# Kernel tuning notes

Hardware: AMD Instinct MI355X
Metric: run time of the kernel (lower is better)

Reference implementation:

```python
import jax, jax.numpy as jnp
import numpy as np

B, D, N, H = 2, 512, 2048, 8
DK = D // H
EPS = 1e-5


def conv1x1(x, w, b):
    # kernel-size-1 Conv1d == channel-mixing GEMM: (o,i) x (b,i,n) -> (b,o,n)
    return jnp.einsum('oi,bin->bon', w, x) + b[None, :, None]


def setup_inputs() -> dict:
    key = jax.random.key(0)
    ks = jax.random.split(key, 20)
    s = 0.02
    return {
        'init_query': jax.random.normal(ks[0], (B, D, N), jnp.float32),
        'key_t': jax.random.normal(ks[1], (B, D, N), jnp.float32),
        'value': jax.random.normal(ks[2], (B, D, N), jnp.float32),
        'mask': jax.random.randint(ks[3], (B, 1, N, N), 0, 2, jnp.int32),
        'Wq': jax.random.normal(ks[4], (D, D), jnp.float32) * s,
        'bq': jax.random.normal(ks[5], (D,), jnp.float32) * s,
        'Wk': jax.random.normal(ks[6], (D, D), jnp.float32) * s,
        'bk': jax.random.normal(ks[7], (D,), jnp.float32) * s,
        'Wv': jax.random.normal(ks[8], (D, D), jnp.float32) * s,
        'bv': jax.random.normal(ks[9], (D,), jnp.float32) * s,
        'Wm': jax.random.normal(ks[10], (D, D), jnp.float32) * s,
        'bm': jax.random.normal(ks[11], (D,), jnp.float32) * s,
        'W1': jax.random.normal(ks[12], (2 * D, 2 * D), jnp.float32) * s,
        'b1': jax.random.normal(ks[13], (2 * D,), jnp.float32) * s,
        'gamma': jnp.ones((2 * D,), jnp.float32),
        'beta': jnp.zeros((2 * D,), jnp.float32),
        'rmean': jax.random.normal(ks[14], (2 * D,), jnp.float32) * s,
        'rvar': jnp.abs(jax.random.normal(ks[15], (2 * D,), jnp.float32)) * 0.1 + 0.5,
        'W2': jax.random.normal(ks[16], (D, 2 * D), jnp.float32) * s,
        'b2': jnp.zeros((D,), jnp.float32),  # nn.init.constant_(bias, 0.0)
    }


def reference(init_query, key_t, value, mask, Wq, bq, Wk, bk, Wv, bv, Wm, bm,
              W1, b1, gamma, beta, rmean, rvar, W2, b2):
    # projections, split channels into (d_k, n_heads) exactly like torch .view
    q = conv1x1(init_query, Wq, bq).reshape(B, DK, H, N)
    k = conv1x1(key_t, Wk, bk).reshape(B, DK, H, N)
    v = conv1x1(value, Wv, bv).reshape(B, DK, H, N)
    scores = jnp.einsum('bdhn,bdhm->bhnm', q, k) / jnp.sqrt(jnp.float32(DK))
    scores = jnp.where(mask == 0, jnp.float32(-1e9), scores)
    attn = jax.nn.softmax(scores, axis=-1)
    x = jnp.einsum('bhnm,bdhm->bdhn', attn, v).reshape(B, D, N)
    x = conv1x1(x, Wm, bm)
    x = jnp.concatenate([x, init_query], axis=1)  # (B, 2D, N)
    h = conv1x1(x, W1, b1)
    # BatchNorm1d (inference mode with running stats) + ReLU
    h = (h - rmean[None, :, None]) * (gamma / jnp.sqrt(rvar + EPS))[None, :, None] + beta[None, :, None]
    h = jax.nn.relu(h)
    return conv1x1(h, W2, b2)
```

## Files before the change

kernel.cpp:

```cpp
#include <hip/hip_runtime.h>

typedef unsigned short u16;
typedef unsigned int u32;
typedef unsigned long long u64;
typedef long long i64;
typedef __bf16 bf16x8 __attribute__((ext_vector_type(8)));
typedef u16 u16x8 __attribute__((ext_vector_type(8)));
typedef u32 u32x2 __attribute__((ext_vector_type(2)));
typedef float f32x4 __attribute__((ext_vector_type(4)));

#define DEV __device__ __forceinline__

constexpr int BB = 2, DD = 512, NN = 2048, HH = 8, DKc = 64, D2 = 1024;

constexpr float QSC = 0.125f * 1.44269504088896340736f;

constexpr i64 OFF_CAT = 0;
constexpr i64 OFF_XKT = 8388608;
constexpr i64 OFF_XVT = 12582912;
constexpr i64 OFF_HT  = 8388608;
constexpr i64 OFF_QH  = 16777216;
constexpr i64 OFF_KH  = 20971520;
constexpr i64 OFF_VT  = 25165824;
constexpr i64 OFF_WQP = 29360128;
constexpr i64 OFF_WKP = 29884416;
constexpr i64 OFF_WVP = 30408704;
constexpr i64 OFF_WMT = 30932992;
constexpr i64 OFF_W1A = 31457280;
constexpr i64 OFF_W1C = 32505856;
constexpr i64 OFF_W2B = 34603008;
constexpr i64 OFF_BQP = 35651584;
constexpr i64 OFF_BKP = 35653632;
constexpr i64 OFF_BVP = 35655680;
constexpr i64 OFF_BNA = 35657728;
constexpr i64 OFF_BNC = 35661824;
constexpr i64 OFF_LP  = 35665920;
constexpr i64 OFF_MSK = 35928064;

DEV u16 f2bf(float f) {
  u32 u = __float_as_uint(f);
  u = u + 0x7FFFu + ((u >> 16) & 1u);
  return (u16)(u >> 16);
}

DEV float bf2f(u16 u) { return __uint_as_float(((u32)u) << 16); }

DEV u32 packbf(float lo, float hi) {
  return __builtin_amdgcn_perm(__float_as_uint(hi), __float_as_uint(lo), 0x07060302u);
}

DEV float fexp2(float x) {
#if __has_builtin(__builtin_amdgcn_exp2f)
  return __builtin_amdgcn_exp2f(x);
#else
  return exp2f(x);
#endif
}

DEV bf16x8 ldfrag(const u16* p) {
  bf16x8 v;
  __builtin_memcpy(&v, __builtin_assume_aligned(p, 16), 16);
  return v;
}

DEV bf16x8 ldfrag8(const u16* p) {
  bf16x8 v;
  __builtin_memcpy(&v, __builtin_assume_aligned(p, 8), 16);
  return v;
}

DEV bf16x8 ones8() {
  u16x8 u = {0x3F80, 0x3F80, 0x3F80, 0x3F80, 0x3F80, 0x3F80, 0x3F80, 0x3F80};
  bf16x8 v;
  __builtin_memcpy(&v, &u, 16);
  return v;
}

DEV void gload16(const void* g, void* lds) {
  __builtin_amdgcn_global_load_lds((__attribute__((address_space(1))) void*)g,
                                   (__attribute__((address_space(3))) void*)lds, 16, 0, 0);
}

DEV f32x4 mfma16(bf16x8 a, bf16x8 b, f32x4 c) {
  return __builtin_amdgcn_mfma_f32_16x16x32_bf16(a, b, c, 0, 0, 0);
}

__global__ __launch_bounds__(256) void prep_kernel(
    const float* __restrict__ Wq, const float* __restrict__ Wk, const float* __restrict__ Wv,
    const float* __restrict__ Wm, const float* __restrict__ W1, const float* __restrict__ W2,
    const float* __restrict__ bq, const float* __restrict__ bk, const float* __restrict__ bv,
    const float* __restrict__ bm, const float* __restrict__ b1, const float* __restrict__ gamma_,
    const float* __restrict__ beta_, const float* __restrict__ rmean,
    const float* __restrict__ rvar, const int* __restrict__ mask,
    u16* __restrict__ wqp, u16* __restrict__ wkp, u16* __restrict__ wvp, u16* __restrict__ wmt,
    u16* __restrict__ w1a, u16* __restrict__ w1c, u16* __restrict__ w2b,
    float* __restrict__ bqp, float* __restrict__ bkp, float* __restrict__ bvp,
    float* __restrict__ bna, float* __restrict__ bnc, u32* __restrict__ mw) {
  const int blk = blockIdx.x, t = threadIdx.x;
  if (blk < 768) {
    const int which = blk >> 8, lb = blk & 255;
    const float* W = which == 0 ? Wq : (which == 1 ? Wk : Wv);
    u16* dst = which == 0 ? wqp : (which == 1 ? wkp : wvp);
    for (int e = lb * 256 + t; e < 262144; e += 65536) {
      int op = e >> 9, i = e & 511;
      int dk = op & 63, h = op >> 6;
      dst[e] = f2bf(W[(dk * 8 + h) * 512 + i]);
    }
  } else if (blk < 1024) {
    const int lb = blk - 768;
    for (int e = lb * 256 + t; e < 262144; e += 65536) {
      int cp = e >> 9, o = e & 511;
      int dk = cp & 63, h = cp >> 6;
      wmt[e] = f2bf(Wm[o * 512 + dk * 8 + h]);
    }
  } else if (blk < 1280) {
    const int lb = blk - 1024;
    for (int e = lb * 256 + t; e < 524288; e += 65536) {
      int row = e >> 9, o = e & 511;
      w1a[e] = f2bf(W1[(i64)row * 1024 + o]);
    }
  } else if (blk < 1536) {
    const int lb = blk - 1280;
    for (int e = lb * 256 + t; e < 524288; e += 65536) {
      int row = e >> 9, j = e & 511;
      w1c[(i64)row * 1024 + 512 + j] = f2bf(W1[(i64)row * 1024 + 512 + j]);
    }
  } else if (blk < 1792) {
    const int lb = blk - 1536;
    for (int e = lb * 256 + t; e < 524288; e += 65536) w2b[e] = f2bf(W2[e]);
  } else if (blk < 1808) {
    __shared__ float sm[4][64];
    const int base = (blk - 1792) * 64;
    const int el = t & 63, oq = t >> 6;
    const float* wrow = W1 + (i64)(base + el) * 1024 + oq * 128;
    const float* bmq = bm + oq * 128;
    float s = 0.f;
#pragma unroll 8
    for (int j = 0; j < 128; j += 4) {
      float4 x = *(const float4*)(wrow + j);
      float4 y = *(const float4*)(bmq + j);
      s += x.x * y.x + x.y * y.y + x.z * y.z + x.w * y.w;
    }
    sm[oq][el] = s;
    __syncthreads();
    if (t < 64) {
      int e = base + t;
      float a = gamma_[e] * rsqrtf(rvar[e] + 1e-5f);
      bna[e] = a;
      bnc[e] = (b1[e] - rmean[e]) * a + beta_[e] + a * (sm[0][t] + sm[1][t] + sm[2][t] + sm[3][t]);
    }
  } else if (blk == 1808) {
    for (int e = t; e < 512; e += 256) {
      int src = (e & 63) * 8 + (e >> 6);
      bqp[e] = bq[src]; bkp[e] = bk[src]; bvp[e] = bv[src];
    }
  } else {
    const int tid = (blk - 1809) * 256 + t;
    const i64 base = (i64)tid * 32;
    const int4* mp = (const int4*)(mask + base);
    u32 word = 0;
#pragma unroll
    for (int j = 0; j < 8; ++j) {
      int4 x = mp[j];
      u32 nib = (x.x != 0 ? 1u : 0u) | (x.y != 0 ? 2u : 0u) | (x.z != 0 ? 4u : 0u) |
                (x.w != 0 ? 8u : 0u);
      word |= nib << (j * 4);
    }
    mw[tid] = word;
  }
}

__global__ __launch_bounds__(256) void transpose_cvt(const float* __restrict__ iq,
                                                     const float* __restrict__ kt,
                                                     const float* __restrict__ vv,
                                                     u16* __restrict__ cat, u16* __restrict__ xkt,
                                                     u16* __restrict__ xvt) {
  __shared__ float tile[32][33];
  const int z = blockIdx.z, tensor = z >> 1, b = z & 1;
  const float* src = tensor == 0 ? iq : (tensor == 1 ? kt : vv);
  src += (i64)b * DD * NN;
  u16* dst; i64 ldd; int coff;
  if (tensor == 0)      { dst = cat + (i64)b * NN * D2; ldd = D2; coff = DD; }
  else if (tensor == 1) { dst = xkt + (i64)b * NN * DD; ldd = DD; coff = 0; }
  else                  { dst = xvt + (i64)b * NN * DD; ldd = DD; coff = 0; }
  const int x0 = blockIdx.x * 32, y0 = blockIdx.y * 32;
  const int col = threadIdx.x & 31, rg = threadIdx.x >> 5;
#pragma unroll
  for (int i = 0; i < 4; ++i) {
    int row = rg + i * 8;
    tile[row][col] = src[(i64)(y0 + row) * NN + x0 + col];
  }
  __syncthreads();
  const int dp = threadIdx.x & 15, rbase = threadIdx.x >> 4;
  u32* dst32 = (u32*)dst;
  const i64 ldw = ldd >> 1;
  const int cw = (coff + y0) >> 1;
#pragma unroll
  for (int i = 0; i < 2; ++i) {
    int rr = rbase + i * 16;
    dst32[(i64)(x0 + rr) * ldw + cw + dp] = packbf(tile[2 * dp][rr], tile[2 * dp + 1][rr]);
  }
}

template <int AM, int AN>
DEV void gemm_core(const u16* __restrict__ A, i64 lda, const u16* __restrict__ Bp, i64 ldb,
                   int K, u16* As, u16* Bs, f32x4 (&acc)[AM][AN]) {
  constexpr int BM = AM * 32, BN = AN * 32;
  const int t = threadIdx.x, w = t >> 6, l = t & 63, quad = l >> 4, l15 = l & 15;
  const int wm = (w >> 1) * AM * 16, wn = (w & 1) * AN * 16;
  for (int kk = 0; kk < K; kk += 64) {
    __syncthreads();
#pragma unroll
    for (int j = 0; j < BM / 32; ++j) {
      int ch = j * 256 + w * 64 + l, r = ch >> 3, c = ch & 7;
      gload16(A + (i64)r * lda + kk + ((c ^ (r & 7)) << 3), As + (j * 256 + w * 64) * 8);
    }
#pragma unroll
    for (int j = 0; j < BN / 32; ++j) {
      int ch = j * 256 + w * 64 + l, r = ch >> 3, c = ch & 7;
      gload16(Bp + (i64)r * ldb + kk + ((c ^ (r & 7)) << 3), Bs + (j * 256 + w * 64) * 8);
    }
    __syncthreads();
#pragma unroll
    for (int kc = 0; kc < 2; ++kc) {
      const int sw = ((kc * 4 + quad) ^ (l15 & 7)) << 3;
      bf16x8 af[AM], bfr[AN];
#pragma unroll
      for (int i = 0; i < AM; ++i) af[i] = ldfrag(&As[(wm + i * 16 + l15) * 64 + sw]);
#pragma unroll
      for (int j = 0; j < AN; ++j) bfr[j] = ldfrag(&Bs[(wn + j * 16 + l15) * 64 + sw]);
#pragma unroll
      for (int i = 0; i < AM; ++i)
#pragma unroll
        for (int j = 0; j < AN; ++j) acc[i][j] = mfma16(af[i], bfr[j], acc[i][j]);
    }
  }
}

__global__ __launch_bounds__(256) void qkv_gemm(const u16* __restrict__ cat,
                                                const u16* __restrict__ xkt,
                                                const u16* __restrict__ xvt,
                                                const u16* __restrict__ wqp,
                                                const u16* __restrict__ wkp,
                                                const u16* __restrict__ wvp,
                                                const float* __restrict__ bqp,
                                                const float* __restrict__ bkp,
                                                const float* __restrict__ bvp,
                                                u16* __restrict__ qh, u16* __restrict__ kh,
                                                u16* __restrict__ vt) {
  __shared__ __align__(16) u16 As[128 * 64];
  __shared__ __align__(16) u16 Bs[64 * 64];
  const int z = blockIdx.z, op = z >> 1, b = z & 1;
  const int t = threadIdx.x, w = t >> 6, l = t & 63, quad = l >> 4, l15 = l & 15;
  const int wm = (w >> 1) * 64, wn = (w & 1) * 32;
  int mx, ny;
  const u16 *A, *Bp;
  i64 lda, ldb;
  if (op < 2) {
    mx = blockIdx.x; ny = blockIdx.y;
    A = (op == 0 ? cat + DD : xkt);
    lda = (op == 0 ? D2 : DD);
    A += (i64)b * NN * lda + (i64)mx * 128 * lda;
    Bp = (op == 0 ? wqp : wkp) + (i64)ny * 64 * DD;
    ldb = DD;
  } else {
    int f = blockIdx.x * 8 + blockIdx.y;
    mx = f >> 5; ny = f & 31;
    A = wvp + (i64)mx * 128 * DD; lda = DD;
    Bp = xvt + (i64)b * NN * DD + (i64)ny * 64 * DD; ldb = DD;
  }
  f32x4 acc[4][2] = {};
  gemm_core<4, 2>(A, lda, Bp, ldb, DD, As, Bs, acc);

  const int rowBase = mx * 128 + wm + quad * 4;
  const int colBase = ny * 64 + wn + l15;
  if (op < 2) {
    const float* bias = (op == 0 ? bqp : bkp);
    const float sc = (op == 0 ? QSC : 1.f);
    u16* dst = (op == 0 ? qh : kh) + (i64)b * HH * NN * DKc;
#pragma unroll
    for (int j = 0; j < 2; ++j) {
      const int col = colBase + j * 16;
      const float cA = bias[col];
#pragma unroll
      for (int i = 0; i < 4; ++i)
#pragma unroll
        for (int r = 0; r < 4; ++r) {
          const int row = rowBase + i * 16 + r;
          dst[(i64)(col >> 6) * (NN * 64) + (i64)row * 64 + (col & 63)] =
              f2bf((acc[i][j][r] + cA) * sc);
        }
    }
  } else {
    u16* dst = vt + (i64)b * HH * DKc * NN;
#pragma unroll
    for (int j = 0; j < 2; ++j) {
      const int col = colBase + j * 16;
      const int colp = (col & ~63) | (((col & 15) << 2) | ((col >> 4) & 3));
#pragma unroll
      for (int i = 0; i < 4; ++i)
#pragma unroll
        for (int r = 0; r < 4; ++r) {
          const int row = rowBase + i * 16 + r;
          dst[(i64)row * NN + colp] = f2bf(acc[i][j][r] + bvp[row]);
        }
    }
  }
}

struct GArgs {
  const u16* A; i64 lda, sAb;
  const u16* B; i64 ldb, sBb;
  void* C; i64 ldc, sCb;
  const float* p1; const float* p2;
  int K;
};

template <int MODE, int AM, int AN>
__global__ __launch_bounds__(256) void gemm_bt(GArgs g) {
  __shared__ __align__(16) u16 As[AM * 32 * 64];
  __shared__ __align__(16) u16 Bs[AN * 32 * 64];
  const int t = threadIdx.x, w = t >> 6, l = t & 63, quad = l >> 4, l15 = l & 15;
  const int wm = (w >> 1) * AM * 16, wn = (w & 1) * AN * 16;
  const int bz = blockIdx.z;
  const u16* A = g.A + (i64)bz * g.sAb + (i64)blockIdx.x * (AM * 32) * g.lda;
  const u16* Bp = g.B + (i64)bz * g.sBb + (i64)blockIdx.y * (AN * 32) * g.ldb;
  f32x4 acc[AM][AN] = {};
  gemm_core<AM, AN>(A, g.lda, Bp, g.ldb, g.K, As, Bs, acc);

  const int rowBase = blockIdx.x * (AM * 32) + wm + quad * 4;
  const int colBase = blockIdx.y * (AN * 32) + wn + l15;
#pragma unroll
  for (int j = 0; j < AN; ++j) {
    const int col = colBase + j * 16;
    float cA = 0.f, cB = 0.f;
    if (MODE == 3) { cA = g.p1[col]; cB = g.p2[col]; }
#pragma unroll
    for (int i = 0; i < AM; ++i) {
#pragma unroll
      for (int r = 0; r < 4; ++r) {
        const int row = rowBase + i * 16 + r;
        float v = acc[i][j][r];
        if (MODE == 3) {
          float x = v * cA + cB;
          ((u16*)g.C + (i64)bz * g.sCb)[(i64)row * g.ldc + col] = f2bf(x > 0.f ? x : 0.f);
        } else if (MODE == 4) {
          ((float*)g.C + (i64)bz * g.sCb)[(i64)row * g.ldc + col] = v + g.p1[row];
        } else {
          ((u16*)g.C + (i64)bz * g.sCb)[(i64)row * g.ldc + col] = f2bf(v);
        }
      }
    }
  }
}

__global__ __launch_bounds__(256) void flash_attn(const u16* __restrict__ Qh,
                                                  const u16* __restrict__ Kh,
                                                  const u16* __restrict__ Vt,
                                                  const u64* __restrict__ MW,
                                                  u16* __restrict__ Opart,
                                                  float* __restrict__ Lp) {
  __shared__ __align__(16) u16 Qs[64 * 64];
  __shared__ __align__(16) u16 Ks[64 * 64];
  __shared__ __align__(16) u16 Vs[64 * 64];
  __shared__ __align__(16) u16 Ps[4][16 * 68];
  const int t = threadIdx.x, w = t >> 6, l = t & 63, quad = l >> 4, l15 = l & 15;
  const int nt = blockIdx.x, h = blockIdx.y, b = blockIdx.z >> 1, sp = blockIdx.z & 1;
  const u16* Qb = Qh + ((i64)(b * HH + h) * NN + nt * 64) * 64;
  const u16* Kb = Kh + (i64)(b * HH + h) * NN * 64;
  const u16* Vb = Vt + (i64)(b * HH + h) * 64 * NN;
  const bf16x8 ONE = ones8();
#pragma unroll
  for (int j = 0; j < 2; ++j) {
    int ch = j * 256 + w * 64 + l, r = ch >> 3, c = ch & 7;
    gload16(Qb + r * 64 + ((c ^ (r & 7)) << 3), &Qs[(j * 256 + w * 64) * 8]);
  }
  __syncthreads();
  bf16x8 qf[2];
#pragma unroll
  for (int kc = 0; kc < 2; ++kc)
    qf[kc] = ldfrag(&Qs[(w * 16 + l15) * 64 + (((kc * 4 + quad) ^ (l15 & 7)) << 3)]);

  f32x4 oacc[4] = {};
  f32x4 lacc = {};
  const int mt0 = sp * 16, mt1 = mt0 + 16;
  for (int mt = mt0; mt < mt1; ++mt) {
    __syncthreads();
#pragma unroll
    for (int j = 0; j < 2; ++j) {
      int ch = j * 256 + w * 64 + l, r = ch >> 3, c = ch & 7;
      gload16(Kb + (i64)mt * 4096 + r * 64 + ((c ^ (r & 7)) << 3), &Ks[(j * 256 + w * 64) * 8]);
      gload16(Vb + (i64)r * NN + mt * 64 + ((c ^ (r & 7)) << 3), &Vs[(j * 256 + w * 64) * 8]);
    }
    __syncthreads();
    f32x4 s[4];
#pragma unroll
    for (int ct = 0; ct < 4; ++ct) {
      const int sw = l15 & 7;
      bf16x8 k0 = ldfrag(&Ks[(ct * 16 + l15) * 64 + ((quad ^ sw) << 3)]);
      bf16x8 k1 = ldfrag(&Ks[(ct * 16 + l15) * 64 + (((4 + quad) ^ sw) << 3)]);
      f32x4 z = {};
      z = mfma16(qf[0], k0, z);
      z = mfma16(qf[1], k1, z);
      s[ct] = z;
    }
#pragma unroll
    for (int r = 0; r < 4; ++r) {
      int n = nt * 64 + w * 16 + quad * 4 + r;
      u64 sh = MW[(i64)(b * NN + n) * 32 + mt] >> l15;
      u32 m01 = ((u32)sh & 0x00010001u) * 0xFFFFu;
      u32 m23 = ((u32)(sh >> 32) & 0x00010001u) * 0xFFFFu;
      u32 w0 = packbf(fexp2(s[0][r]), fexp2(s[1][r])) & m01;
      u32 w1 = packbf(fexp2(s[2][r]), fexp2(s[3][r])) & m23;
      u32x2 pair = {w0, w1};
      __builtin_memcpy(__builtin_assume_aligned(&Ps[w][(quad * 4 + r) * 68 + l15 * 4], 8), &pair, 8);
    }
    asm volatile("" ::: "memory");
    bf16x8 pf0 = ldfrag8(&Ps[w][l15 * 68 + quad * 8]);
    bf16x8 pf1 = ldfrag8(&Ps[w][l15 * 68 + 32 + quad * 8]);
    lacc = mfma16(pf0, ONE, lacc);
    lacc = mfma16(pf1, ONE, lacc);
#pragma unroll
    for (int dt = 0; dt < 4; ++dt) {
      const int sw = l15 & 7;
      bf16x8 v0 = ldfrag(&Vs[(dt * 16 + l15) * 64 + ((quad ^ sw) << 3)]);
      bf16x8 v1 = ldfrag(&Vs[(dt * 16 + l15) * 64 + (((4 + quad) ^ sw) << 3)]);
      oacc[dt] = mfma16(pf0, v0, oacc[dt]);
      oacc[dt] = mfma16(pf1, v1, oacc[dt]);
    }
  }
  u16* Op = Opart + (i64)sp * BB * NN * DD;
#pragma unroll
  for (int dt = 0; dt < 4; ++dt)
#pragma unroll
    for (int r = 0; r < 4; ++r) {
      int n = nt * 64 + w * 16 + quad * 4 + r;
      Op[((i64)b * NN + n) * DD + h * DKc + dt * 16 + l15] = f2bf(oacc[dt][r]);
    }
  if (l15 == 0) {
#pragma unroll
    for (int r = 0; r < 4; ++r) {
      int n = nt * 64 + w * 16 + quad * 4 + r;
      Lp[((i64)(sp * BB + b) * HH + h) * NN + n] = lacc[r];
    }
  }
}

__global__ __launch_bounds__(256) void combine(const u16* __restrict__ Opart,
                                               const float* __restrict__ Lp,
                                               u16* __restrict__ cat) {
  const int tid = blockIdx.x * 256 + threadIdx.x;
  const int b = tid >> 18, rem = tid & 262143;
  const int n = rem >> 7, cq = rem & 127;
  const int c0 = cq << 2, h = c0 >> 6;
  const u16* p0 = Opart + ((i64)b * NN + n) * DD + c0;
  const u16* p1 = p0 + (i64)BB * NN * DD;
  u16 a0[4], a1[4];
  __builtin_memcpy(a0, __builtin_assume_aligned(p0, 8), 8);
  __builtin_memcpy(a1, __builtin_assume_aligned(p1, 8), 8);
  float l0 = Lp[((i64)b * HH + h) * NN + n];
  float l1 = Lp[((i64)(BB + b) * HH + h) * NN + n];
  float rl = __builtin_amdgcn_rcpf(l0 + l1);
  u16 o[4];
#pragma unroll
  for (int j = 0; j < 4; ++j) o[j] = f2bf((bf2f(a0[j]) + bf2f(a1[j])) * rl);
  __builtin_memcpy(__builtin_assume_aligned(&cat[((i64)b * NN + n) * D2 + c0], 8), o, 8);
}

extern "C" void kernel_launch(void* const* d_in, const int* in_sizes, int n_in,
                              void* d_out, int out_size, void* d_ws, size_t ws_size,
                              hipStream_t stream) {
  (void)in_sizes; (void)n_in; (void)out_size; (void)ws_size;
  const float* iq    = (const float*)d_in[0];
  const float* kt    = (const float*)d_in[1];
  const float* vv    = (const float*)d_in[2];
  const int*   mask  = (const int*)d_in[3];
  const float* Wq    = (const float*)d_in[4];
  const float* bq    = (const float*)d_in[5];
  const float* Wk    = (const float*)d_in[6];
  const float* bk    = (const float*)d_in[7];
  const float* Wv    = (const float*)d_in[8];
  const float* bv    = (const float*)d_in[9];
  const float* Wm    = (const float*)d_in[10];
  const float* bm    = (const float*)d_in[11];
  const float* W1    = (const float*)d_in[12];
  const float* b1    = (const float*)d_in[13];
  const float* gamma_= (const float*)d_in[14];
  const float* beta_ = (const float*)d_in[15];
  const float* rmean = (const float*)d_in[16];
  const float* rvar  = (const float*)d_in[17];
  const float* W2    = (const float*)d_in[18];
  const float* b2    = (const float*)d_in[19];

  char* ws = (char*)d_ws;
  u16* cat = (u16*)(ws + OFF_CAT);
  u16* xkt = (u16*)(ws + OFF_XKT);
  u16* xvt = (u16*)(ws + OFF_XVT);
  u16* ht  = (u16*)(ws + OFF_HT);
  u16* qh  = (u16*)(ws + OFF_QH);
  u16* kh  = (u16*)(ws + OFF_KH);
  u16* vt  = (u16*)(ws + OFF_VT);
  u16* wqp = (u16*)(ws + OFF_WQP);
  u16* wkp = (u16*)(ws + OFF_WKP);
  u16* wvp = (u16*)(ws + OFF_WVP);
  u16* wmt = (u16*)(ws + OFF_WMT);
  u16* w1a = (u16*)(ws + OFF_W1A);
  u16* w1c = (u16*)(ws + OFF_W1C);
  u16* w2b = (u16*)(ws + OFF_W2B);
  float* bqp = (float*)(ws + OFF_BQP);
  float* bkp = (float*)(ws + OFF_BKP);
  float* bvp = (float*)(ws + OFF_BVP);
  float* bna = (float*)(ws + OFF_BNA);
  float* bnc = (float*)(ws + OFF_BNC);
  float* lp  = (float*)(ws + OFF_LP);
  u32* mw = (u32*)(ws + OFF_MSK);
  u16* opart = (u16*)(ws + OFF_XKT);

  prep_kernel<<<2833, 256, 0, stream>>>(Wq, Wk, Wv, Wm, W1, W2, bq, bk, bv, bm, b1, gamma_,
                                        beta_, rmean, rvar, mask, wqp, wkp, wvp, wmt, w1a, w1c,
                                        w2b, bqp, bkp, bvp, bna, bnc, mw);
  transpose_cvt<<<dim3(64, 16, 6), 256, 0, stream>>>(iq, kt, vv, cat, xkt, xvt);

  GArgs ca{w1a, DD, 0, wmt, DD, 0, w1c, D2, 0, nullptr, nullptr, DD};
  gemm_bt<5, 4, 2><<<dim3(8, 8, 1), 256, 0, stream>>>(ca);

  qkv_gemm<<<dim3(16, 8, 6), 256, 0, stream>>>(cat, xkt, xvt, wqp, wkp, wvp, bqp, bkp, bvp,
                                               qh, kh, vt);

  flash_attn<<<dim3(32, 8, 4), 256, 0, stream>>>(qh, kh, vt, (const u64*)mw, opart, lp);
  combine<<<2048, 256, 0, stream>>>(opart, lp, cat);

  GArgs wa{cat, D2, (i64)NN * D2, w1c, D2, 0, ht, D2, (i64)NN * D2, bna, bnc, D2};
  gemm_bt<3, 4, 2><<<dim3(16, 16, 2), 256, 0, stream>>>(wa);
  GArgs w2a{w2b, D2, 0, ht, D2, (i64)NN * D2, d_out, NN, (i64)DD * NN, b2, nullptr, D2};
  gemm_bt<4, 2, 2><<<dim3(8, 32, 2), 256, 0, stream>>>(w2a);
}
```

Before: 237.9 us.

## Merge prep kernels, fold Wm·W1 GEMM into QKV launch, use 32x32 MFMA attention with 4-way split

Fuses the prep and transpose kernels into a single launch, and folds the W1·Wm weight-composition GEMM into the QKV GEMM launch as an extra z-slice. Flash attention is rewritten to use 32x32x16 MFMA with 128-row query tiles, Q fragments loaded straight from global memory, and a 4-way KV split. The mask bitpacking and V column permutation are changed to match the new fragment layout, and the combine kernel now sums four partials. The workspace is re-laid out so the partial outputs no longer alias the transposed inputs, and the W1 GEMM tile shape is changed. The goal is fewer launches and higher MFMA efficiency, at the cost of more partial-output traffic and a strided mask gather.

```diff
diff --git a/kernel.cpp b/kernel.cpp
--- a/kernel.cpp
+++ b/kernel.cpp
@@ -6,8 +6,8 @@
 typedef long long i64;
 typedef __bf16 bf16x8 __attribute__((ext_vector_type(8)));
 typedef u16 u16x8 __attribute__((ext_vector_type(8)));
-typedef u32 u32x2 __attribute__((ext_vector_type(2)));
 typedef float f32x4 __attribute__((ext_vector_type(4)));
+typedef float f32x16 __attribute__((ext_vector_type(16)));
 
 #define DEV __device__ __forceinline__
 
@@ -15,27 +15,29 @@
 
 constexpr float QSC = 0.125f * 1.44269504088896340736f;
 
+constexpr i64 MB = 1048576;
 constexpr i64 OFF_CAT = 0;
-constexpr i64 OFF_XKT = 8388608;
-constexpr i64 OFF_XVT = 12582912;
-constexpr i64 OFF_HT  = 8388608;
-constexpr i64 OFF_QH  = 16777216;
-constexpr i64 OFF_KH  = 20971520;
-constexpr i64 OFF_VT  = 25165824;
-constexpr i64 OFF_WQP = 29360128;
-constexpr i64 OFF_WKP = 29884416;
-constexpr i64 OFF_WVP = 30408704;
-constexpr i64 OFF_WMT = 30932992;
-constexpr i64 OFF_W1A = 31457280;
-constexpr i64 OFF_W1C = 32505856;
-constexpr i64 OFF_W2B = 34603008;
-constexpr i64 OFF_BQP = 35651584;
-constexpr i64 OFF_BKP = 35653632;
-constexpr i64 OFF_BVP = 35655680;
-constexpr i64 OFF_BNA = 35657728;
-constexpr i64 OFF_BNC = 35661824;
-constexpr i64 OFF_LP  = 35665920;
-constexpr i64 OFF_MSK = 35928064;
+constexpr i64 OFF_XKT = 8 * MB;
+constexpr i64 OFF_XVT = 12 * MB;
+constexpr i64 OFF_QH  = 16 * MB;
+constexpr i64 OFF_KH  = 20 * MB;
+constexpr i64 OFF_VT  = 24 * MB;
+constexpr i64 OFF_HT  = 28 * MB;
+constexpr i64 OFF_OP  = 36 * MB;
+constexpr i64 OFF_LP  = 68 * MB;
+constexpr i64 OFF_WQP = 69 * MB;
+constexpr i64 OFF_WKP = 69 * MB + 524288;
+constexpr i64 OFF_WVP = 69 * MB + 1048576;
+constexpr i64 OFF_WMT = 69 * MB + 1572864;
+constexpr i64 OFF_W1A = 71 * MB;
+constexpr i64 OFF_W1C = 72 * MB;
+constexpr i64 OFF_W2B = 74 * MB;
+constexpr i64 OFF_BQP = 75 * MB;
+constexpr i64 OFF_BKP = 75 * MB + 2048;
+constexpr i64 OFF_BVP = 75 * MB + 4096;
+constexpr i64 OFF_BNA = 75 * MB + 8192;
+constexpr i64 OFF_BNC = 75 * MB + 12288;
+constexpr i64 OFF_MSK = 76 * MB;
 
 DEV u16 f2bf(float f) {
   u32 u = __float_as_uint(f);
@@ -85,17 +87,24 @@
   return __builtin_amdgcn_mfma_f32_16x16x32_bf16(a, b, c, 0, 0, 0);
 }
 
-__global__ __launch_bounds__(256) void prep_kernel(
+DEV f32x16 mfma32(bf16x8 a, bf16x8 b, f32x16 c) {
+  return __builtin_amdgcn_mfma_f32_32x32x16_bf16(a, b, c, 0, 0, 0);
+}
+
+__global__ __launch_bounds__(256) void prep_all(
     const float* __restrict__ Wq, const float* __restrict__ Wk, const float* __restrict__ Wv,
     const float* __restrict__ Wm, const float* __restrict__ W1, const float* __restrict__ W2,
     const float* __restrict__ bq, const float* __restrict__ bk, const float* __restrict__ bv,
     const float* __restrict__ bm, const float* __restrict__ b1, const float* __restrict__ gamma_,
     const float* __restrict__ beta_, const float* __restrict__ rmean,
     const float* __restrict__ rvar, const int* __restrict__ mask,
+    const float* __restrict__ iq, const float* __restrict__ kt, const float* __restrict__ vv,
     u16* __restrict__ wqp, u16* __restrict__ wkp, u16* __restrict__ wvp, u16* __restrict__ wmt,
     u16* __restrict__ w1a, u16* __restrict__ w1c, u16* __restrict__ w2b,
     float* __restrict__ bqp, float* __restrict__ bkp, float* __restrict__ bvp,
-    float* __restrict__ bna, float* __restrict__ bnc, u32* __restrict__ mw) {
+    float* __restrict__ bna, float* __restrict__ bnc, u32* __restrict__ mw,
+    u16* __restrict__ cat, u16* __restrict__ xkt, u16* __restrict__ xvt) {
+  __shared__ float tile[32][33];
   const int blk = blockIdx.x, t = threadIdx.x;
   if (blk < 768) {
     const int which = blk >> 8, lb = blk & 255;
@@ -154,51 +163,44 @@
       int src = (e & 63) * 8 + (e >> 6);
       bqp[e] = bq[src]; bkp[e] = bk[src]; bvp[e] = bv[src];
     }
+  } else if (blk < 2833) {
+    const int tid = (blk - 1809) * 256 + t;
+    const int l = tid & 63, mt = (tid >> 6) & 31, g = (tid >> 11) & 63, b = tid >> 17;
+    const int kv0 = mt * 64 + (l & 31);
+    u32 word = 0;
+#pragma unroll
+    for (int reg = 0; reg < 16; ++reg) {
+      int r = (reg & 3) + 8 * (reg >> 2) + 4 * (l >> 5);
+      const int* mp = mask + ((i64)b * NN + g * 32 + r) * NN + kv0;
+      word |= (mp[0] != 0 ? (1u << (2 * reg)) : 0u) | (mp[32] != 0 ? (2u << (2 * reg)) : 0u);
+    }
+    mw[tid] = word;
   } else {
-    const int tid = (blk - 1809) * 256 + t;
-    const i64 base = (i64)tid * 32;
-    const int4* mp = (const int4*)(mask + base);
-    u32 word = 0;
-#pragma unroll
-    for (int j = 0; j < 8; ++j) {
-      int4 x = mp[j];
-      u32 nib = (x.x != 0 ? 1u : 0u) | (x.y != 0 ? 2u : 0u) | (x.z != 0 ? 4u : 0u) |
-                (x.w != 0 ? 8u : 0u);
-      word |= nib << (j * 4);
-    }
-    mw[tid] = word;
-  }
-}
-
-__global__ __launch_bounds__(256) void transpose_cvt(const float* __restrict__ iq,
-                                                     const float* __restrict__ kt,
-                                                     const float* __restrict__ vv,
-                                                     u16* __restrict__ cat, u16* __restrict__ xkt,
-                                                     u16* __restrict__ xvt) {
-  __shared__ float tile[32][33];
-  const int z = blockIdx.z, tensor = z >> 1, b = z & 1;
-  const float* src = tensor == 0 ? iq : (tensor == 1 ? kt : vv);
-  src += (i64)b * DD * NN;
-  u16* dst; i64 ldd; int coff;
-  if (tensor == 0)      { dst = cat + (i64)b * NN * D2; ldd = D2; coff = DD; }
-  else if (tensor == 1) { dst = xkt + (i64)b * NN * DD; ldd = DD; coff = 0; }
-  else                  { dst = xvt + (i64)b * NN * DD; ldd = DD; coff = 0; }
-  const int x0 = blockIdx.x * 32, y0 = blockIdx.y * 32;
-  const int col = threadIdx.x & 31, rg = threadIdx.x >> 5;
-#pragma unroll
-  for (int i = 0; i < 4; ++i) {
-    int row = rg + i * 8;
-    tile[row][col] = src[(i64)(y0 + row) * NN + x0 + col];
-  }
-  __syncthreads();
-  const int dp = threadIdx.x & 15, rbase = threadIdx.x >> 4;
-  u32* dst32 = (u32*)dst;
-  const i64 ldw = ldd >> 1;
-  const int cw = (coff + y0) >> 1;
-#pragma unroll
-  for (int i = 0; i < 2; ++i) {
-    int rr = rbase + i * 16;
-    dst32[(i64)(x0 + rr) * ldw + cw + dp] = packbf(tile[2 * dp][rr], tile[2 * dp + 1][rr]);
+    const int idx = blk - 2833;
+    const int bx = idx & 63, by = (idx >> 6) & 15, bz = idx >> 10;
+    const int tensor = bz >> 1, b = bz & 1;
+    const float* src = (tensor == 0 ? iq : (tensor == 1 ? kt : vv)) + (i64)b * DD * NN;
+    u16* dst; i64 ldd; int coff;
+    if (tensor == 0)      { dst = cat + (i64)b * NN * D2; ldd = D2; coff = DD; }
+    else if (tensor == 1) { dst = xkt + (i64)b * NN * DD; ldd = DD; coff = 0; }
+    else                  { dst = xvt + (i64)b * NN * DD; ldd = DD; coff = 0; }
+    const int x0 = bx * 32, y0 = by * 32;
+    const int col = t & 31, rg = t >> 5;
+#pragma unroll
+    for (int i = 0; i < 4; ++i) {
+      int row = rg + i * 8;
+      tile[row][col] = src[(i64)(y0 + row) * NN + x0 + col];
+    }
+    __syncthreads();
+    const int dp = t & 15, rbase = t >> 4;
+    u32* dst32 = (u32*)dst;
+    const i64 ldw = ldd >> 1;
+    const int cw = (coff + y0) >> 1;
+#pragma unroll
+    for (int i = 0; i < 2; ++i) {
+      int rr = rbase + i * 16;
+      dst32[(i64)(x0 + rr) * ldw + cw + dp] = packbf(tile[2 * dp][rr], tile[2 * dp + 1][rr]);
+    }
   }
 }
 
@@ -243,14 +245,17 @@
                                                 const u16* __restrict__ wqp,
                                                 const u16* __restrict__ wkp,
                                                 const u16* __restrict__ wvp,
+                                                const u16* __restrict__ w1a,
+                                                const u16* __restrict__ wmt,
                                                 const float* __restrict__ bqp,
                                                 const float* __restrict__ bkp,
                                                 const float* __restrict__ bvp,
                                                 u16* __restrict__ qh, u16* __restrict__ kh,
-                                                u16* __restrict__ vt) {
+                                                u16* __restrict__ vt, u16* __restrict__ w1c) {
   __shared__ __align__(16) u16 As[128 * 64];
   __shared__ __align__(16) u16 Bs[64 * 64];
-  const int z = blockIdx.z, op = z >> 1, b = z & 1;
+  const int z = blockIdx.z, b = z & 1;
+  const int op = (z == 6) ? 3 : (z >> 1);
   const int t = threadIdx.x, w = t >> 6, l = t & 63, quad = l >> 4, l15 = l & 15;
   const int wm = (w >> 1) * 64, wn = (w & 1) * 32;
   int mx, ny;
@@ -263,11 +268,16 @@
     A += (i64)b * NN * lda + (i64)mx * 128 * lda;
     Bp = (op == 0 ? wqp : wkp) + (i64)ny * 64 * DD;
     ldb = DD;
-  } else {
+  } else if (op == 2) {
     int f = blockIdx.x * 8 + blockIdx.y;
     mx = f >> 5; ny = f & 31;
     A = wvp + (i64)mx * 128 * DD; lda = DD;
     Bp = xvt + (i64)b * NN * DD + (i64)ny * 64 * DD; ldb = DD;
+  } else {
+    if (blockIdx.x >= 8) return;
+    mx = blockIdx.x; ny = blockIdx.y;
+    A = w1a + (i64)mx * 128 * DD; lda = DD;
+    Bp = wmt + (i64)ny * 64 * DD; ldb = DD;
   }
   f32x4 acc[4][2] = {};
   gemm_core<4, 2>(A, lda, Bp, ldb, DD, As, Bs, acc);
@@ -291,18 +301,30 @@
               f2bf((acc[i][j][r] + cA) * sc);
         }
     }
-  } else {
+  } else if (op == 2) {
     u16* dst = vt + (i64)b * HH * DKc * NN;
 #pragma unroll
     for (int j = 0; j < 2; ++j) {
       const int col = colBase + j * 16;
-      const int colp = (col & ~63) | (((col & 15) << 2) | ((col >> 4) & 3));
+      const int colp = (col & ~63) | (((col & 31) << 1) | ((col >> 5) & 1));
 #pragma unroll
       for (int i = 0; i < 4; ++i)
 #pragma unroll
         for (int r = 0; r < 4; ++r) {
           const int row = rowBase + i * 16 + r;
           dst[(i64)row * NN + colp] = f2bf(acc[i][j][r] + bvp[row]);
+        }
+    }
+  } else {
+#pragma unroll
+    for (int j = 0; j < 2; ++j) {
+      const int col = colBase + j * 16;
+#pragma unroll
+      for (int i = 0; i < 4; ++i)
+#pragma unroll
+        for (int r = 0; r < 4; ++r) {
+          const int row = rowBase + i * 16 + r;
+          w1c[(i64)row * D2 + col] = f2bf(acc[i][j][r]);
         }
     }
   }
@@ -344,10 +366,8 @@
         if (MODE == 3) {
           float x = v * cA + cB;
           ((u16*)g.C + (i64)bz * g.sCb)[(i64)row * g.ldc + col] = f2bf(x > 0.f ? x : 0.f);
-        } else if (MODE == 4) {
+        } else {
           ((float*)g.C + (i64)bz * g.sCb)[(i64)row * g.ldc + col] = v + g.p1[row];
-        } else {
-          ((u16*)g.C + (i64)bz * g.sCb)[(i64)row * g.ldc + col] = f2bf(v);
         }
       }
     }
@@ -357,92 +377,79 @@
 __global__ __launch_bounds__(256) void flash_attn(const u16* __restrict__ Qh,
                                                   const u16* __restrict__ Kh,
                                                   const u16* __restrict__ Vt,
-                                                  const u64* __restrict__ MW,
+                                                  const u32* __restrict__ MW2,
                                                   u16* __restrict__ Opart,
                                                   float* __restrict__ Lp) {
-  __shared__ __align__(16) u16 Qs[64 * 64];
   __shared__ __align__(16) u16 Ks[64 * 64];
   __shared__ __align__(16) u16 Vs[64 * 64];
-  __shared__ __align__(16) u16 Ps[4][16 * 68];
-  const int t = threadIdx.x, w = t >> 6, l = t & 63, quad = l >> 4, l15 = l & 15;
-  const int nt = blockIdx.x, h = blockIdx.y, b = blockIdx.z >> 1, sp = blockIdx.z & 1;
-  const u16* Qb = Qh + ((i64)(b * HH + h) * NN + nt * 64) * 64;
+  __shared__ __align__(16) u16 Ps[4][32 * 68];
+  const int t = threadIdx.x, w = t >> 6, l = t & 63, l31 = l & 31, lh = l >> 5;
+  const int nt = blockIdx.x, h = blockIdx.y, b = blockIdx.z >> 2, sp = blockIdx.z & 3;
+  const u16* Qb = Qh + ((i64)(b * HH + h) * NN + nt * 128 + w * 32) * 64;
   const u16* Kb = Kh + (i64)(b * HH + h) * NN * 64;
   const u16* Vb = Vt + (i64)(b * HH + h) * 64 * NN;
+  const u32* MWb = MW2 + ((i64)(b * 64 + nt * 4 + w) * 32) * 64 + l;
   const bf16x8 ONE = ones8();
-#pragma unroll
-  for (int j = 0; j < 2; ++j) {
-    int ch = j * 256 + w * 64 + l, r = ch >> 3, c = ch & 7;
-    gload16(Qb + r * 64 + ((c ^ (r & 7)) << 3), &Qs[(j * 256 + w * 64) * 8]);
-  }
-  __syncthreads();
-  bf16x8 qf[2];
-#pragma unroll
-  for (int kc = 0; kc < 2; ++kc)
-    qf[kc] = ldfrag(&Qs[(w * 16 + l15) * 64 + (((kc * 4 + quad) ^ (l15 & 7)) << 3)]);
-
-  f32x4 oacc[4] = {};
-  f32x4 lacc = {};
-  const int mt0 = sp * 16, mt1 = mt0 + 16;
-  for (int mt = mt0; mt < mt1; ++mt) {
+  bf16x8 qf[4];
+#pragma unroll
+  for (int kc = 0; kc < 4; ++kc)
+    __builtin_memcpy(&qf[kc], Qb + (i64)l31 * 64 + kc * 16 + lh * 8, 16);
+
+  f32x16 oacc0 = {}, oacc1 = {}, lacc = {};
+  for (int mt = sp * 8; mt < sp * 8 + 8; ++mt) {
     __syncthreads();
 #pragma unroll
     for (int j = 0; j < 2; ++j) {
-      int ch = j * 256 + w * 64 + l, r = ch >> 3, c = ch & 7;
-      gload16(Kb + (i64)mt * 4096 + r * 64 + ((c ^ (r & 7)) << 3), &Ks[(j * 256 + w * 64) * 8]);
-      gload16(Vb + (i64)r * NN + mt * 64 + ((c ^ (r & 7)) << 3), &Vs[(j * 256 + w * 64) * 8]);
+      int ch = j * 256 + t, r = ch >> 3, c = ch & 7;
+      gload16(Kb + (i64)(mt * 64 + r) * 64 + ((c ^ (r & 7)) << 3), &Ks[ch * 8]);
+      gload16(Vb + (i64)r * NN + mt * 64 + ((c ^ (r & 7)) << 3), &Vs[ch * 8]);
     }
     __syncthreads();
-    f32x4 s[4];
-#pragma unroll
-    for (int ct = 0; ct < 4; ++ct) {
-      const int sw = l15 & 7;
-      bf16x8 k0 = ldfrag(&Ks[(ct * 16 + l15) * 64 + ((quad ^ sw) << 3)]);
-      bf16x8 k1 = ldfrag(&Ks[(ct * 16 + l15) * 64 + (((4 + quad) ^ sw) << 3)]);
-      f32x4 z = {};
-      z = mfma16(qf[0], k0, z);
-      z = mfma16(qf[1], k1, z);
-      s[ct] = z;
-    }
-#pragma unroll
-    for (int r = 0; r < 4; ++r) {
-      int n = nt * 64 + w * 16 + quad * 4 + r;
-      u64 sh = MW[(i64)(b * NN + n) * 32 + mt] >> l15;
-      u32 m01 = ((u32)sh & 0x00010001u) * 0xFFFFu;
-      u32 m23 = ((u32)(sh >> 32) & 0x00010001u) * 0xFFFFu;
-      u32 w0 = packbf(fexp2(s[0][r]), fexp2(s[1][r])) & m01;
-      u32 w1 = packbf(fexp2(s[2][r]), fexp2(s[3][r])) & m23;
-      u32x2 pair = {w0, w1};
-      __builtin_memcpy(__builtin_assume_aligned(&Ps[w][(quad * 4 + r) * 68 + l15 * 4], 8), &pair, 8);
+    f32x16 s0 = {}, s1 = {};
+#pragma unroll
+    for (int kc = 0; kc < 4; ++kc) {
+      const int r1 = 32 + l31;
+      bf16x8 k0 = ldfrag(&Ks[l31 * 64 + (((kc * 2 + lh) ^ (l31 & 7)) << 3)]);
+      bf16x8 k1 = ldfrag(&Ks[r1 * 64 + (((kc * 2 + lh) ^ (r1 & 7)) << 3)]);
+      s0 = mfma32(qf[kc], k0, s0);
+      s1 = mfma32(qf[kc], k1, s1);
+    }
+    const u32 mword = MWb[(i64)mt * 64];
+#pragma unroll
+    for (int reg = 0; reg < 16; ++reg) {
+      const int row = (reg & 3) + 8 * (reg >> 2) + 4 * lh;
+      u32 sh = mword >> (2 * reg);
+      u32 m01 = ((sh & 1u) | ((sh & 2u) << 15)) * 0xFFFFu;
+      u32 pv = packbf(fexp2(s0[reg]), fexp2(s1[reg])) & m01;
+      *(u32*)__builtin_assume_aligned(&Ps[w][row * 68 + l31 * 2], 4) = pv;
     }
     asm volatile("" ::: "memory");
-    bf16x8 pf0 = ldfrag8(&Ps[w][l15 * 68 + quad * 8]);
-    bf16x8 pf1 = ldfrag8(&Ps[w][l15 * 68 + 32 + quad * 8]);
-    lacc = mfma16(pf0, ONE, lacc);
-    lacc = mfma16(pf1, ONE, lacc);
-#pragma unroll
-    for (int dt = 0; dt < 4; ++dt) {
-      const int sw = l15 & 7;
-      bf16x8 v0 = ldfrag(&Vs[(dt * 16 + l15) * 64 + ((quad ^ sw) << 3)]);
-      bf16x8 v1 = ldfrag(&Vs[(dt * 16 + l15) * 64 + (((4 + quad) ^ sw) << 3)]);
-      oacc[dt] = mfma16(pf0, v0, oacc[dt]);
-      oacc[dt] = mfma16(pf1, v1, oacc[dt]);
-    }
-  }
-  u16* Op = Opart + (i64)sp * BB * NN * DD;
-#pragma unroll
-  for (int dt = 0; dt < 4; ++dt)
-#pragma unroll
-    for (int r = 0; r < 4; ++r) {
-      int n = nt * 64 + w * 16 + quad * 4 + r;
-      Op[((i64)b * NN + n) * DD + h * DKc + dt * 16 + l15] = f2bf(oacc[dt][r]);
-    }
-  if (l15 == 0) {
-#pragma unroll
-    for (int r = 0; r < 4; ++r) {
-      int n = nt * 64 + w * 16 + quad * 4 + r;
-      Lp[((i64)(sp * BB + b) * HH + h) * NN + n] = lacc[r];
-    }
+    bf16x8 pf[4];
+#pragma unroll
+    for (int kc = 0; kc < 4; ++kc) pf[kc] = ldfrag8(&Ps[w][l31 * 68 + kc * 16 + lh * 8]);
+#pragma unroll
+    for (int kc = 0; kc < 4; ++kc) lacc = mfma32(pf[kc], ONE, lacc);
+#pragma unroll
+    for (int kc = 0; kc < 4; ++kc) {
+      const int r1 = 32 + l31;
+      bf16x8 v0 = ldfrag(&Vs[l31 * 64 + (((kc * 2 + lh) ^ (l31 & 7)) << 3)]);
+      bf16x8 v1 = ldfrag(&Vs[r1 * 64 + (((kc * 2 + lh) ^ (r1 & 7)) << 3)]);
+      oacc0 = mfma32(pf[kc], v0, oacc0);
+      oacc1 = mfma32(pf[kc], v1, oacc1);
+    }
+  }
+  u16* Op = Opart + (i64)sp * (BB * NN * DD) + ((i64)b * NN + nt * 128 + w * 32) * DD + h * 64;
+#pragma unroll
+  for (int reg = 0; reg < 16; ++reg) {
+    const int row = (reg & 3) + 8 * (reg >> 2) + 4 * lh;
+    Op[(i64)row * DD + l31] = f2bf(oacc0[reg]);
+    Op[(i64)row * DD + 32 + l31] = f2bf(oacc1[reg]);
+  }
+  if (l31 == 0) {
+    float* Lpb = Lp + ((i64)(sp * BB + b) * HH + h) * NN + nt * 128 + w * 32;
+#pragma unroll
+    for (int reg = 0; reg < 16; ++reg)
+      Lpb[(reg & 3) + 8 * (reg >> 2) + 4 * lh] = lacc[reg];
   }
 }
 
@@ -453,17 +460,22 @@
   const int b = tid >> 18, rem = tid & 262143;
   const int n = rem >> 7, cq = rem & 127;
   const int c0 = cq << 2, h = c0 >> 6;
-  const u16* p0 = Opart + ((i64)b * NN + n) * DD + c0;
-  const u16* p1 = p0 + (i64)BB * NN * DD;
-  u16 a0[4], a1[4];
-  __builtin_memcpy(a0, __builtin_assume_aligned(p0, 8), 8);
-  __builtin_memcpy(a1, __builtin_assume_aligned(p1, 8), 8);
-  float l0 = Lp[((i64)b * HH + h) * NN + n];
-  float l1 = Lp[((i64)(BB + b) * HH + h) * NN + n];
-  float rl = __builtin_amdgcn_rcpf(l0 + l1);
+  const i64 base = ((i64)b * NN + n) * DD + c0;
+  const i64 stride = (i64)BB * NN * DD;
+  float acc[4] = {0.f, 0.f, 0.f, 0.f};
+  float lsum = 0.f;
+#pragma unroll
+  for (int s = 0; s < 4; ++s) {
+    u16 a[4];
+    __builtin_memcpy(a, __builtin_assume_aligned(Opart + s * stride + base, 8), 8);
+#pragma unroll
+    for (int j = 0; j < 4; ++j) acc[j] += bf2f(a[j]);
+    lsum += Lp[((i64)(s * BB + b) * HH + h) * NN + n];
+  }
+  float rl = __builtin_amdgcn_rcpf(lsum);
   u16 o[4];
 #pragma unroll
-  for (int j = 0; j < 4; ++j) o[j] = f2bf((bf2f(a0[j]) + bf2f(a1[j])) * rl);
+  for (int j = 0; j < 4; ++j) o[j] = f2bf(acc[j] * rl);
   __builtin_memcpy(__builtin_assume_aligned(&cat[((i64)b * NN + n) * D2 + c0], 8), o, 8);
 }
 
@@ -496,10 +508,12 @@
   u16* cat = (u16*)(ws + OFF_CAT);
   u16* xkt = (u16*)(ws + OFF_XKT);
   u16* xvt = (u16*)(ws + OFF_XVT);
-  u16* ht  = (u16*)(ws + OFF_HT);
   u16* qh  = (u16*)(ws + OFF_QH);
   u16* kh  = (u16*)(ws + OFF_KH);
   u16* vt  = (u16*)(ws + OFF_VT);
+  u16* ht  = (u16*)(ws + OFF_HT);
+  u16* opart = (u16*)(ws + OFF_OP);
+  float* lp  = (float*)(ws + OFF_LP);
   u16* wqp = (u16*)(ws + OFF_WQP);
   u16* wkp = (u16*)(ws + OFF_WKP);
   u16* wvp = (u16*)(ws + OFF_WVP);
@@ -512,26 +526,17 @@
   float* bvp = (float*)(ws + OFF_BVP);
   float* bna = (float*)(ws + OFF_BNA);
   float* bnc = (float*)(ws + OFF_BNC);
-  float* lp  = (float*)(ws + OFF_LP);
   u32* mw = (u32*)(ws + OFF_MSK);
-  u16* opart = (u16*)(ws + OFF_XKT);
-
-  prep_kernel<<<2833, 256, 0, stream>>>(Wq, Wk, Wv, Wm, W1, W2, bq, bk, bv, bm, b1, gamma_,
-                                        beta_, rmean, rvar, mask, wqp, wkp, wvp, wmt, w1a, w1c,
-                                        w2b, bqp, bkp, bvp, bna, bnc, mw);
-  transpose_cvt<<<dim3(64, 16, 6), 256, 0, stream>>>(iq, kt, vv, cat, xkt, xvt);
-
-  GArgs ca{w1a, DD, 0, wmt, DD, 0, w1c, D2, 0, nullptr, nullptr, DD};
-  gemm_bt<5, 4, 2><<<dim3(8, 8, 1), 256, 0, stream>>>(ca);
-
-  qkv_gemm<<<dim3(16, 8, 6), 256, 0, stream>>>(cat, xkt, xvt, wqp, wkp, wvp, bqp, bkp, bvp,
-                                               qh, kh, vt);
-
-  flash_attn<<<dim3(32, 8, 4), 256, 0, stream>>>(qh, kh, vt, (const u64*)mw, opart, lp);
+
+  prep_all<<<8977, 256, 0, stream>>>(Wq, Wk, Wv, Wm, W1, W2, bq, bk, bv, bm, b1, gamma_, beta_,
+                                     rmean, rvar, mask, iq, kt, vv, wqp, wkp, wvp, wmt, w1a, w1c,
+                                     w2b, bqp, bkp, bvp, bna, bnc, mw, cat, xkt, xvt);
+  qkv_gemm<<<dim3(16, 8, 7), 256, 0, stream>>>(cat, xkt, xvt, wqp, wkp, wvp, w1a, wmt,
+                                               bqp, bkp, bvp, qh, kh, vt, w1c);
+  flash_attn<<<dim3(16, 8, 8), 256, 0, stream>>>(qh, kh, vt, mw, opart, lp);
   combine<<<2048, 256, 0, stream>>>(opart, lp, cat);
-
   GArgs wa{cat, D2, (i64)NN * D2, w1c, D2, 0, ht, D2, (i64)NN * D2, bna, bnc, D2};
-  gemm_bt<3, 4, 2><<<dim3(16, 16, 2), 256, 0, stream>>>(wa);
+  gemm_bt<3, 2, 2><<<dim3(32, 16, 2), 256, 0, stream>>>(wa);
   GArgs w2a{w2b, D2, 0, ht, D2, (i64)NN * D2, d_out, NN, (i64)DD * NN, b2, nullptr, D2};
   gemm_bt<4, 2, 2><<<dim3(8, 32, 2), 256, 0, stream>>>(w2a);
 }
```

Measured after the change: 219.0 us. -8.0%, faster.
